# Kernel tuning notes

Hardware: AMD Instinct MI355X
Metric: run time of the kernel (lower is better)

The kernel has to match this reference:

```python
import jax, jax.numpy as jnp
import numpy as np

N = 50000      # nodes
E = 800000     # edges
F_IN = 256     # feat_dim
H = 256        # hidden dim (both layers)
L = 128        # latent dim
BN_EPS = 1e-5


def setup_inputs() -> dict:
    key = jax.random.key(0)
    ks = jax.random.split(key, 16)
    x = jax.random.normal(ks[0], (N, F_IN), dtype=jnp.float32)
    edge_index = jax.random.randint(ks[1], (2, E), 0, N, dtype=jnp.int32)
    s = 0.05
    return {
        "x": x,
        "edge_index": edge_index,
        "W0": s * jax.random.normal(ks[2], (F_IN, H), jnp.float32),
        "b0": jnp.zeros((H,), jnp.float32),
        "gamma0": jnp.ones((H,), jnp.float32),
        "beta0": jnp.zeros((H,), jnp.float32),
        "W1": s * jax.random.normal(ks[3], (H, H), jnp.float32),
        "b1": jnp.zeros((H,), jnp.float32),
        "gamma1": jnp.ones((H,), jnp.float32),
        "beta1": jnp.zeros((H,), jnp.float32),
        "W_mu": s * jax.random.normal(ks[4], (H, L), jnp.float32),
        "b_mu": jnp.zeros((L,), jnp.float32),
        "W_lv": s * jax.random.normal(ks[5], (H, L), jnp.float32),
        "b_lv": jnp.zeros((L,), jnp.float32),
    }


def _gcn_conv(h, src, dst, coef, W, b):
    # h' = W h, then symmetric-normalized scatter-add aggregation (PyG GCNConv)
    h = h @ W                                   # [N, H]
    msg = h[src] * coef                         # gather + scale, [E+N, H]
    out = jax.ops.segment_sum(msg, dst, num_segments=N)
    return out + b


def _bn(h, gamma, beta):
    # BatchNorm1d over node dimension (training-mode batch statistics)
    m = h.mean(axis=0)
    v = h.var(axis=0)
    return (h - m) * jax.lax.rsqrt(v + BN_EPS) * gamma + beta


def reference(x, edge_index, W0, b0, gamma0, beta0, W1, b1, gamma1, beta1,
              W_mu, b_mu, W_lv, b_lv):
    loops = jnp.arange(N, dtype=edge_index.dtype)
    src = jnp.concatenate([edge_index[0], loops])   # with self-loops
    dst = jnp.concatenate([edge_index[1], loops])
    deg = jax.ops.segment_sum(jnp.ones((E + N,), x.dtype), dst, num_segments=N)
    dinv = jnp.where(deg > 0, jax.lax.rsqrt(jnp.maximum(deg, 1.0)), 0.0)
    coef = (dinv[src] * dinv[dst])[:, None]          # [E+N, 1]

    h = jax.nn.relu(_bn(_gcn_conv(x, src, dst, coef, W0, b0), gamma0, beta0))
    h = jax.nn.relu(_bn(_gcn_conv(h, src, dst, coef, W1, b1), gamma1, beta1))
    # dropout is identity at inference
    mu = h @ W_mu + b_mu
    logvar = h @ W_lv + b_lv
    return mu, logvar
```

## Files before the change

kernel.cpp:

```cpp
#include <hip/hip_runtime.h>
#include <hip/hip_bf16.h>

#define NN 50000
#define NP 50001
#define NE 800000
#define FD 256
#define LD 128
#define BN_EPS 1e-5f
#define NEPAD (NE + 7 * NN + 16)

typedef __bf16 bf16_t;
typedef bf16_t bf16x8 __attribute__((ext_vector_type(8)));
typedef float f32x4 __attribute__((ext_vector_type(4)));
typedef float f32x2 __attribute__((ext_vector_type(2)));
typedef int i32x2 __attribute__((ext_vector_type(2)));
typedef int i32x4 __attribute__((ext_vector_type(4)));
typedef unsigned int u32x4 __attribute__((ext_vector_type(4)));
typedef unsigned short u16x8 __attribute__((ext_vector_type(8)));


__global__ __launch_bounds__(256) void k_count(const int* __restrict__ dst,
                                               int* __restrict__ cnt) {
  int i = blockIdx.x * blockDim.x + threadIdx.x;
  if (i < NE) atomicAdd(&cnt[dst[i]], 1);
}

__global__ __launch_bounds__(256) void k_scanA(const int* __restrict__ cnt,
                                               int* __restrict__ row_ptr,
                                               int* __restrict__ partials) {
  __shared__ int ws[4];
  int b = blockIdx.x, t = threadIdx.x;
  int base = b * 1024 + t * 4;
  int vals[4];
#pragma unroll
  for (int j = 0; j < 4; ++j)
    vals[j] = (base + j < NN) ? ((cnt[base + j] + 7) & ~7) : 0;
  int tsum = vals[0] + vals[1] + vals[2] + vals[3];
  int lane = t & 63, wid = t >> 6;
  int x = tsum;
#pragma unroll
  for (int off = 1; off < 64; off <<= 1) {
    int y = __shfl_up(x, off, 64);
    if (lane >= off) x += y;
  }
  if (lane == 63) ws[wid] = x;
  __syncthreads();
  int woff = 0;
  for (int w = 0; w < wid; ++w) woff += ws[w];
  int run = woff + x - tsum;
#pragma unroll
  for (int j = 0; j < 4; ++j) {
    if (base + j < NN) row_ptr[base + j] = run;
    run += vals[j];
  }
  if (t == 255) partials[b] = woff + x;
}

__global__ void k_scanB(int* __restrict__ partials, int* __restrict__ row_ptr,
                        int nblk) {
  int lane = threadIdx.x;
  int v = (lane < nblk) ? partials[lane] : 0;
  int x = v;
#pragma unroll
  for (int off = 1; off < 64; off <<= 1) {
    int y = __shfl_up(x, off, 64);
    if (lane >= off) x += y;
  }
  if (lane < nblk) partials[lane] = x - v;
  if (lane == nblk - 1) row_ptr[NN] = x;
}

__global__ __launch_bounds__(256) void k_scanC(int* __restrict__ row_ptr,
                                               const int* __restrict__ partials,
                                               const int* __restrict__ cnt,
                                               float* __restrict__ dinv,
                                               unsigned short* __restrict__ col,
                                               int* __restrict__ hist) {
  __shared__ int lh[64];
  int b = blockIdx.x, t = threadIdx.x;
  if (t < 64) lh[t] = 0;
  __syncthreads();
  int off = partials[b];
  int base = b * 1024 + t * 4;
#pragma unroll
  for (int j = 0; j < 4; ++j)
    if (base + j < NN) {
      int deg = cnt[base + j];
      int rp = row_ptr[base + j] + off;
      row_ptr[base + j] = rp;
      dinv[base + j] = rsqrtf(1.0f + (float)deg);
      int pd = (deg + 7) & ~7;
      for (int p = deg; p < pd; ++p) col[rp + p] = (unsigned short)NN;
      int it = pd >> 3;
      if (it > 63) it = 63;
      atomicAdd(&lh[it], 1);
    }
  __syncthreads();
  if (t < 64 && lh[t]) atomicAdd(&hist[t], lh[t]);
}

__global__ __launch_bounds__(256) void k_fill(const int* __restrict__ src,
                                              const int* __restrict__ dst,
                                              const int* __restrict__ row_ptr,
                                              int* __restrict__ cursor,
                                              unsigned short* __restrict__ col) {
  int i = blockIdx.x * blockDim.x + threadIdx.x;
  if (i < NE) {
    int d = dst[i];
    int p = atomicAdd(&cursor[d], 1);
    col[row_ptr[d] + p] = (unsigned short)src[i];
  }
}

__global__ void k_hscan(const int* __restrict__ hist, int* __restrict__ binoff) {
  int l = threadIdx.x;
  int v = hist[l];
  int x = v;
#pragma unroll
  for (int off = 1; off < 64; off <<= 1) {
    int y = __shfl_up(x, off, 64);
    if (l >= off) x += y;
  }
  binoff[l] = x - v;
}

__global__ __launch_bounds__(256) void k_order(
    const int* __restrict__ cnt, const int* __restrict__ row_ptr,
    const float* __restrict__ dinv, int* __restrict__ binoff,
    int* __restrict__ order, i32x2* __restrict__ desc,
    float* __restrict__ dinvp) {
  __shared__ int lcnt[64];
  __shared__ int gbase[64];
  int t = threadIdx.x;
  if (t < 64) lcnt[t] = 0;
  __syncthreads();
  int i = blockIdx.x * 256 + t;
  int it = 0, rloc = 0, pd = 0;
  bool valid = (i < NN);
  if (valid) {
    pd = (cnt[i] + 7) & ~7;
    it = pd >> 3;
    if (it > 63) it = 63;
    rloc = atomicAdd(&lcnt[it], 1);
  }
  __syncthreads();
  if (t < 64 && lcnt[t]) gbase[t] = atomicAdd(&binoff[t], lcnt[t]);
  __syncthreads();
  if (valid) {
    int p = gbase[it] + rloc;
    order[p] = i;
    int rp = row_ptr[i];
    desc[p] = (i32x2){rp, rp + pd};
    dinvp[p] = dinv[i];
  }
}

__global__ __launch_bounds__(256) void k_convw(
    const float* __restrict__ W0, const float* __restrict__ W1,
    const float* __restrict__ Wmu, const float* __restrict__ bmu,
    const float* __restrict__ Wlv, const float* __restrict__ blv,
    bf16_t* __restrict__ W0s, bf16_t* __restrict__ W1s,
    bf16_t* __restrict__ Whs, float* __restrict__ biash,
    bf16_t* __restrict__ g16, bf16_t* __restrict__ agg16) {
  int k = blockIdx.x, n = threadIdx.x;
  int chunk = (n >> 4) * 8 + (k >> 5);
  int slot = ((k >> 3) & 3) * 16 + (n & 15);
  int idx = chunk * 512 + slot * 8 + (k & 7);
  W0s[idx] = (bf16_t)W0[k * 256 + n];
  W1s[idx] = (bf16_t)W1[k * 256 + n];
  float wh = (n < 128) ? Wmu[k * 128 + n] : Wlv[k * 128 + (n - 128)];
  Whs[idx] = (bf16_t)wh;
  if (k == 0) biash[n] = (n < 128) ? bmu[n] : blv[n - 128];
  if (k == 1) {
    int ss = n >> 6, j = n & 63;
    g16[((size_t)ss * NP + NN) * 64 + j] = (bf16_t)0.f;
    agg16[((size_t)ss * NP + NN) * 64 + j] = (bf16_t)0.f;
  }
}

__global__ __launch_bounds__(256) void k_mgemm(
    const void* __restrict__ Ap, int a_f32, const bf16_t* __restrict__ Wswz,
    bf16_t* __restrict__ Cb, float* __restrict__ Cf, int M,
    const float* __restrict__ stats, const float* __restrict__ gamma,
    const float* __restrict__ beta, const float* __restrict__ row_scale,
    const float* __restrict__ col_bias, int split) {
  __shared__ bf16_t Ws[64 * 512];
  __shared__ float bnsc_l[256], bnsh_l[256];
  const int tid = threadIdx.x;
  const int half = blockIdx.y;
  {
    const bf16_t* srcW = Wswz + (size_t)half * 64 * 512;
    bf16x8 wraw[16];
#pragma unroll
    for (int i = 0; i < 16; ++i)
      wraw[i] = *(const bf16x8*)&srcW[(i * 256 + tid) * 8];
#pragma unroll
    for (int i = 0; i < 16; ++i) *(bf16x8*)&Ws[(i * 256 + tid) * 8] = wraw[i];
  }
  if (stats) {
    float mean = stats[tid] * (1.0f / NN);
    float var = stats[256 + tid] * (1.0f / NN) - mean * mean;
    float rs = rsqrtf(var + BN_EPS);
    float sc = gamma[tid] * rs;
    bnsc_l[tid] = sc;
    bnsh_l[tid] = beta[tid] - mean * sc;
  }
  __syncthreads();

  const int wave = tid >> 6, lane = tid & 63;
  const int m = lane & 15, q = lane >> 4;
  const int row0 = blockIdx.x * 128 + wave * 32;
  const int rg0 = row0 + m, rg1 = row0 + 16 + m;
  const int rc0 = rg0 < M ? rg0 : M - 1;
  const int rc1 = rg1 < M ? rg1 : M - 1;

  bf16x8 af[2][8];
  if (a_f32) {
    const float* p0 = (const float*)Ap + (size_t)rc0 * 256 + q * 8;
    const float* p1 = (const float*)Ap + (size_t)rc1 * 256 + q * 8;
#pragma unroll
    for (int g = 0; g < 2; ++g) {
      const float* p = g ? p1 : p0;
      float4 f0[8], f1[8];
#pragma unroll
      for (int kb = 0; kb < 8; ++kb) {
        f0[kb] = *(const float4*)(p + kb * 32);
        f1[kb] = *(const float4*)(p + kb * 32 + 4);
      }
#pragma unroll
      for (int kb = 0; kb < 8; ++kb) {
        bf16x8 fr;
        fr[0] = (bf16_t)f0[kb].x; fr[1] = (bf16_t)f0[kb].y;
        fr[2] = (bf16_t)f0[kb].z; fr[3] = (bf16_t)f0[kb].w;
        fr[4] = (bf16_t)f1[kb].x; fr[5] = (bf16_t)f1[kb].y;
        fr[6] = (bf16_t)f1[kb].z; fr[7] = (bf16_t)f1[kb].w;
        af[g][kb] = fr;
      }
    }
  } else {
    const bf16_t* pA = (const bf16_t*)Ap;
    bf16x8 raw[16];
#pragma unroll
    for (int kb = 0; kb < 8; ++kb) {
      raw[kb * 2 + 0] = *(const bf16x8*)&pA[((size_t)(kb >> 1) * NP + rc0) * 64 +
                                            (kb & 1) * 32 + q * 8];
      raw[kb * 2 + 1] = *(const bf16x8*)&pA[((size_t)(kb >> 1) * NP + rc1) * 64 +
                                            (kb & 1) * 32 + q * 8];
    }
#pragma unroll
    for (int kb = 0; kb < 8; ++kb) {
      float s[8], h[8];
      if (stats) {
        float4 s0 = *(const float4*)&bnsc_l[kb * 32 + q * 8];
        float4 s1 = *(const float4*)&bnsc_l[kb * 32 + q * 8 + 4];
        float4 h0 = *(const float4*)&bnsh_l[kb * 32 + q * 8];
        float4 h1 = *(const float4*)&bnsh_l[kb * 32 + q * 8 + 4];
        s[0] = s0.x; s[1] = s0.y; s[2] = s0.z; s[3] = s0.w;
        s[4] = s1.x; s[5] = s1.y; s[6] = s1.z; s[7] = s1.w;
        h[0] = h0.x; h[1] = h0.y; h[2] = h0.z; h[3] = h0.w;
        h[4] = h1.x; h[5] = h1.y; h[6] = h1.z; h[7] = h1.w;
      }
#pragma unroll
      for (int g = 0; g < 2; ++g) {
        bf16x8 r = raw[kb * 2 + g];
        bf16x8 fr;
#pragma unroll
        for (int j = 0; j < 8; ++j) {
          float v = (float)r[j];
          if (stats) v = fmaxf(fmaf(v, s[j], h[j]), 0.f);
          fr[j] = (bf16_t)v;
        }
        af[g][kb] = fr;
      }
    }
  }

  f32x4 acc[2][8] = {};
#pragma unroll
  for (int nt = 0; nt < 8; ++nt) {
#pragma unroll
    for (int kb = 0; kb < 8; ++kb) {
      bf16x8 b = *(const bf16x8*)&Ws[(nt * 8 + kb) * 512 + lane * 8];
      acc[0][nt] = __builtin_amdgcn_mfma_f32_16x16x32_bf16(af[0][kb], b,
                                                           acc[0][nt], 0, 0, 0);
      acc[1][nt] = __builtin_amdgcn_mfma_f32_16x16x32_bf16(af[1][kb], b,
                                                           acc[1][nt], 0, 0, 0);
    }
  }

#pragma unroll
  for (int g = 0; g < 2; ++g) {
#pragma unroll
    for (int r = 0; r < 4; ++r) {
      int row = row0 + g * 16 + q * 4 + r;
      if (row >= M) continue;
      float rs = row_scale ? row_scale[row] : 1.0f;
#pragma unroll
      for (int nt = 0; nt < 8; ++nt) {
        int col = half * 128 + nt * 16 + m;
        float v = acc[g][nt][r] * rs;
        if (col_bias) v += col_bias[col];
        if (Cb) {
          Cb[((size_t)(col >> 6) * NP + row) * 64 + (col & 63)] = (bf16_t)v;
        } else if (!split) {
          Cf[(size_t)row * 256 + col] = v;
        } else {
          if (col < 128)
            Cf[(size_t)row * 128 + col] = v;
          else
            Cf[(size_t)(M + row) * 128 + (col - 128)] = v;
        }
      }
    }
  }
}

#define ACCUM8(A, d)                                             \
  A[0] += (f32x2){__uint_as_float(d[0] << 16),                   \
                  __uint_as_float(d[0] & 0xffff0000u)};          \
  A[1] += (f32x2){__uint_as_float(d[1] << 16),                   \
                  __uint_as_float(d[1] & 0xffff0000u)};          \
  A[2] += (f32x2){__uint_as_float(d[2] << 16),                   \
                  __uint_as_float(d[2] & 0xffff0000u)};          \
  A[3] += (f32x2){__uint_as_float(d[3] << 16),                   \
                  __uint_as_float(d[3] & 0xffff0000u)};

__global__ __launch_bounds__(256) void k_spmm(
    const bf16_t* __restrict__ g, const int* __restrict__ order,
    const i32x2* __restrict__ desc, const unsigned short* __restrict__ col,
    const float* __restrict__ dinvp, bf16_t* __restrict__ out,
    float* __restrict__ stats) {
  __shared__ float sbuf[32][64];
  const int s = blockIdx.x & 3;
  const int grp = blockIdx.x >> 2;
  const int team = threadIdx.x >> 3, tl = threadIdx.x & 7;
  const int slotA = grp * 64 + team * 2;
  const u32x4* gu = (const u32x4*)(g + (size_t)s * NP * 64);
  float s1[8] = {}, s2[8] = {};
  if (slotA < NN) {
    f32x2 accA[4] = {}, accB[4] = {};
    i32x2 o2 = *(const i32x2*)&order[slotA];
    i32x4 d4 = *(const i32x4*)&desc[slotA];
    f32x2 dv2 = *(const f32x2*)&dinvp[slotA];
    int dstA = o2[0], dstB = o2[1];
    int bA = d4[0], eA = d4[1], bB = d4[2], eB = d4[3];
    {
      u32x4 dA = gu[(size_t)dstA * 8 + tl];
      u32x4 dB = gu[(size_t)dstB * 8 + tl];
      ACCUM8(accA, dA)
      ACCUM8(accB, dB)
    }
    u16x8 cA = {}, cB = {};
    if (bA < eA) cA = __builtin_nontemporal_load((const u16x8*)&col[bA]);
    if (bB < eB) cB = __builtin_nontemporal_load((const u16x8*)&col[bB]);
    while (bA < eA && bB < eB) {
      u32x4 wa0 = gu[(size_t)cA[0] * 8 + tl];
      u32x4 wa1 = gu[(size_t)cA[1] * 8 + tl];
      u32x4 wa2 = gu[(size_t)cA[2] * 8 + tl];
      u32x4 wa3 = gu[(size_t)cA[3] * 8 + tl];
      u32x4 wa4 = gu[(size_t)cA[4] * 8 + tl];
      u32x4 wa5 = gu[(size_t)cA[5] * 8 + tl];
      u32x4 wa6 = gu[(size_t)cA[6] * 8 + tl];
      u32x4 wa7 = gu[(size_t)cA[7] * 8 + tl];
      u32x4 wb0 = gu[(size_t)cB[0] * 8 + tl];
      u32x4 wb1 = gu[(size_t)cB[1] * 8 + tl];
      u32x4 wb2 = gu[(size_t)cB[2] * 8 + tl];
      u32x4 wb3 = gu[(size_t)cB[3] * 8 + tl];
      u32x4 wb4 = gu[(size_t)cB[4] * 8 + tl];
      u32x4 wb5 = gu[(size_t)cB[5] * 8 + tl];
      u32x4 wb6 = gu[(size_t)cB[6] * 8 + tl];
      u32x4 wb7 = gu[(size_t)cB[7] * 8 + tl];
      int bnA = bA + 8, bnB = bB + 8;
      u16x8 cnA = {}, cnB = {};
      if (bnA < eA) cnA = __builtin_nontemporal_load((const u16x8*)&col[bnA]);
      if (bnB < eB) cnB = __builtin_nontemporal_load((const u16x8*)&col[bnB]);
      ACCUM8(accA, wa0) ACCUM8(accA, wa1) ACCUM8(accA, wa2) ACCUM8(accA, wa3)
      ACCUM8(accA, wa4) ACCUM8(accA, wa5) ACCUM8(accA, wa6) ACCUM8(accA, wa7)
      ACCUM8(accB, wb0) ACCUM8(accB, wb1) ACCUM8(accB, wb2) ACCUM8(accB, wb3)
      ACCUM8(accB, wb4) ACCUM8(accB, wb5) ACCUM8(accB, wb6) ACCUM8(accB, wb7)
      cA = cnA;
      cB = cnB;
      bA = bnA;
      bB = bnB;
    }
    while (bA < eA) {
      u32x4 w0 = gu[(size_t)cA[0] * 8 + tl];
      u32x4 w1 = gu[(size_t)cA[1] * 8 + tl];
      u32x4 w2 = gu[(size_t)cA[2] * 8 + tl];
      u32x4 w3 = gu[(size_t)cA[3] * 8 + tl];
      u32x4 w4 = gu[(size_t)cA[4] * 8 + tl];
      u32x4 w5 = gu[(size_t)cA[5] * 8 + tl];
      u32x4 w6 = gu[(size_t)cA[6] * 8 + tl];
      u32x4 w7 = gu[(size_t)cA[7] * 8 + tl];
      int bn = bA + 8;
      u16x8 cn = {};
      if (bn < eA) cn = __builtin_nontemporal_load((const u16x8*)&col[bn]);
      ACCUM8(accA, w0) ACCUM8(accA, w1) ACCUM8(accA, w2) ACCUM8(accA, w3)
      ACCUM8(accA, w4) ACCUM8(accA, w5) ACCUM8(accA, w6) ACCUM8(accA, w7)
      cA = cn;
      bA = bn;
    }
    while (bB < eB) {
      u32x4 w0 = gu[(size_t)cB[0] * 8 + tl];
      u32x4 w1 = gu[(size_t)cB[1] * 8 + tl];
      u32x4 w2 = gu[(size_t)cB[2] * 8 + tl];
      u32x4 w3 = gu[(size_t)cB[3] * 8 + tl];
      u32x4 w4 = gu[(size_t)cB[4] * 8 + tl];
      u32x4 w5 = gu[(size_t)cB[5] * 8 + tl];
      u32x4 w6 = gu[(size_t)cB[6] * 8 + tl];
      u32x4 w7 = gu[(size_t)cB[7] * 8 + tl];
      int bn = bB + 8;
      u16x8 cn = {};
      if (bn < eB) cn = __builtin_nontemporal_load((const u16x8*)&col[bn]);
      ACCUM8(accB, w0) ACCUM8(accB, w1) ACCUM8(accB, w2) ACCUM8(accB, w3)
      ACCUM8(accB, w4) ACCUM8(accB, w5) ACCUM8(accB, w6) ACCUM8(accB, w7)
      cB = cn;
      bB = bn;
    }
    float dvA = dv2[0], dvB = dv2[1];
    bf16x8 ovA, ovB;
#pragma unroll
    for (int j = 0; j < 8; ++j) {
      ovA[j] = (bf16_t)(accA[j >> 1][j & 1] * dvA);
      ovB[j] = (bf16_t)(accB[j >> 1][j & 1] * dvB);
    }
    __builtin_nontemporal_store(
        ovA, (bf16x8*)&out[((size_t)s * NP + dstA) * 64 + (size_t)tl * 8]);
    __builtin_nontemporal_store(
        ovB, (bf16x8*)&out[((size_t)s * NP + dstB) * 64 + (size_t)tl * 8]);
#pragma unroll
    for (int j = 0; j < 8; ++j) {
      float va = (float)ovA[j], vb = (float)ovB[j];
      s1[j] += va + vb;
      s2[j] = fmaf(va, va, s2[j]);
      s2[j] = fmaf(vb, vb, s2[j]);
    }
  }
#pragma unroll
  for (int j = 0; j < 8; ++j) sbuf[team][tl * 8 + j] = s1[j];
  __syncthreads();
  if (threadIdx.x < 64) {
    float tot = 0.f;
#pragma unroll
    for (int w = 0; w < 32; ++w) tot += sbuf[w][threadIdx.x];
    atomicAdd(&stats[s * 64 + threadIdx.x], tot);
  }
  __syncthreads();
#pragma unroll
  for (int j = 0; j < 8; ++j) sbuf[team][tl * 8 + j] = s2[j];
  __syncthreads();
  if (threadIdx.x < 64) {
    float tot = 0.f;
#pragma unroll
    for (int w = 0; w < 32; ++w) tot += sbuf[w][threadIdx.x];
    atomicAdd(&stats[256 + s * 64 + threadIdx.x], tot);
  }
}

extern "C" void kernel_launch(void* const* d_in, const int* in_sizes, int n_in,
                              void* d_out, int out_size, void* d_ws, size_t ws_size,
                              hipStream_t stream) {
  const float* x = (const float*)d_in[0];
  const int* ei = (const int*)d_in[1];
  const int* esrc = ei;
  const int* edst = ei + NE;
  const float* W0 = (const float*)d_in[2];
  const float* gamma0 = (const float*)d_in[4];
  const float* beta0 = (const float*)d_in[5];
  const float* W1 = (const float*)d_in[6];
  const float* gamma1 = (const float*)d_in[8];
  const float* beta1 = (const float*)d_in[9];
  const float* W_mu = (const float*)d_in[10];
  const float* b_mu = (const float*)d_in[11];
  const float* W_lv = (const float*)d_in[12];
  const float* b_lv = (const float*)d_in[13];
  float* out = (float*)d_out;

  bf16_t* g16 = (bf16_t*)d_ws;
  bf16_t* agg16 = g16 + (size_t)4 * NP * 64;
  int* cnt = (int*)(agg16 + (size_t)4 * NP * 64);
  int* cursor = cnt + NN;
  float* statsAll = (float*)(cursor + NN);
  int* hist = (int*)(statsAll + 1024);
  int* binoff = hist + 64;
  float* dinv = (float*)(binoff + 64);
  float* biash = dinv + NN;
  bf16_t* W0s = (bf16_t*)(biash + 256);
  bf16_t* W1s = W0s + 256 * 256;
  bf16_t* Whs = W1s + 256 * 256;
  int* row_ptr = (int*)(Whs + 256 * 256);
  int* order = row_ptr + NN + 4;
  float* dinvp = (float*)(order + NN);
  i32x2* desc = (i32x2*)(dinvp + NN);
  unsigned short* col = (unsigned short*)(desc + NN);
  int* partials = (int*)(col + NEPAD);

  const int SCAN_BLKS = (NN + 1023) / 1024;

  hipMemsetAsync(cnt, 0, (2 * NN + 1024 + 128) * sizeof(int), stream);
  k_count<<<(NE + 255) / 256, 256, 0, stream>>>(edst, cnt);
  k_scanA<<<SCAN_BLKS, 256, 0, stream>>>(cnt, row_ptr, partials);
  k_scanB<<<1, 64, 0, stream>>>(partials, row_ptr, SCAN_BLKS);
  k_scanC<<<SCAN_BLKS, 256, 0, stream>>>(row_ptr, partials, cnt, dinv, col,
                                         hist);
  k_fill<<<(NE + 255) / 256, 256, 0, stream>>>(esrc, edst, row_ptr, cursor, col);
  k_hscan<<<1, 64, 0, stream>>>(hist, binoff);
  k_order<<<(NN + 255) / 256, 256, 0, stream>>>(cnt, row_ptr, dinv, binoff,
                                                order, desc, dinvp);
  k_convw<<<256, 256, 0, stream>>>(W0, W1, W_mu, b_mu, W_lv, b_lv, W0s, W1s,
                                   Whs, biash, g16, agg16);

  dim3 gg((NN + 127) / 128, 2);
  const int SPMM_BLKS = 4 * ((NN + 63) / 64);

  k_mgemm<<<gg, 256, 0, stream>>>(x, 1, W0s, g16, nullptr, NN, nullptr, nullptr,
                                  nullptr, dinv, nullptr, 0);
  k_spmm<<<SPMM_BLKS, 256, 0, stream>>>(g16, order, desc, col, dinvp, agg16,
                                        statsAll);

  k_mgemm<<<gg, 256, 0, stream>>>(agg16, 0, W1s, g16, nullptr, NN, statsAll,
                                  gamma0, beta0, dinv, nullptr, 0);
  k_spmm<<<SPMM_BLKS, 256, 0, stream>>>(g16, order, desc, col, dinvp, agg16,
                                        statsAll + 512);

  k_mgemm<<<gg, 256, 0, stream>>>(agg16, 0, Whs, nullptr, out, NN,
                                  statsAll + 512, gamma1, beta1, nullptr, biash,
                                  1);
}
```

Before: 410.8 us.

## Drop LDS weight staging in GEMM, halve row tile, fold hist scan into order

The GEMM kernel no longer stages its 64KB weight half in shared memory. Each lane now reads B fragments straight from global memory (L2-resident), and each wave handles 16 rows instead of 32, with twice as many blocks. This removes the large LDS footprint and the sync that limited occupancy, at the cost of repeated global/L2 weight reads and less reuse of each B fragment. Separately, the single-wave histogram scan kernel is folded into k_order, where every block recomputes the 64-bin prefix and uses a separate rank counter, which saves one launch.

```diff
diff --git a/kernel.cpp b/kernel.cpp
--- a/kernel.cpp
+++ b/kernel.cpp
@@ -112,27 +112,26 @@
   }
 }
 
-__global__ void k_hscan(const int* __restrict__ hist, int* __restrict__ binoff) {
-  int l = threadIdx.x;
-  int v = hist[l];
-  int x = v;
-#pragma unroll
-  for (int off = 1; off < 64; off <<= 1) {
-    int y = __shfl_up(x, off, 64);
-    if (l >= off) x += y;
-  }
-  binoff[l] = x - v;
-}
-
 __global__ __launch_bounds__(256) void k_order(
     const int* __restrict__ cnt, const int* __restrict__ row_ptr,
-    const float* __restrict__ dinv, int* __restrict__ binoff,
-    int* __restrict__ order, i32x2* __restrict__ desc,
+    const float* __restrict__ dinv, const int* __restrict__ hist,
+    int* __restrict__ rank, int* __restrict__ order, i32x2* __restrict__ desc,
     float* __restrict__ dinvp) {
   __shared__ int lcnt[64];
   __shared__ int gbase[64];
+  __shared__ int sc[64];
   int t = threadIdx.x;
-  if (t < 64) lcnt[t] = 0;
+  if (t < 64) {
+    lcnt[t] = 0;
+    int v = hist[t];
+    int x = v;
+#pragma unroll
+    for (int off = 1; off < 64; off <<= 1) {
+      int y = __shfl_up(x, off, 64);
+      if (t >= off) x += y;
+    }
+    sc[t] = x - v;
+  }
   __syncthreads();
   int i = blockIdx.x * 256 + t;
   int it = 0, rloc = 0, pd = 0;
@@ -144,7 +143,7 @@
     rloc = atomicAdd(&lcnt[it], 1);
   }
   __syncthreads();
-  if (t < 64 && lcnt[t]) gbase[t] = atomicAdd(&binoff[t], lcnt[t]);
+  if (t < 64 && lcnt[t]) gbase[t] = sc[t] + atomicAdd(&rank[t], lcnt[t]);
   __syncthreads();
   if (valid) {
     int p = gbase[it] + rloc;
@@ -184,19 +183,9 @@
     const float* __restrict__ stats, const float* __restrict__ gamma,
     const float* __restrict__ beta, const float* __restrict__ row_scale,
     const float* __restrict__ col_bias, int split) {
-  __shared__ bf16_t Ws[64 * 512];
   __shared__ float bnsc_l[256], bnsh_l[256];
   const int tid = threadIdx.x;
   const int half = blockIdx.y;
-  {
-    const bf16_t* srcW = Wswz + (size_t)half * 64 * 512;
-    bf16x8 wraw[16];
-#pragma unroll
-    for (int i = 0; i < 16; ++i)
-      wraw[i] = *(const bf16x8*)&srcW[(i * 256 + tid) * 8];
-#pragma unroll
-    for (int i = 0; i < 16; ++i) *(bf16x8*)&Ws[(i * 256 + tid) * 8] = wraw[i];
-  }
   if (stats) {
     float mean = stats[tid] * (1.0f / NN);
     float var = stats[256 + tid] * (1.0f / NN) - mean * mean;
@@ -204,49 +193,40 @@
     float sc = gamma[tid] * rs;
     bnsc_l[tid] = sc;
     bnsh_l[tid] = beta[tid] - mean * sc;
-  }
-  __syncthreads();
+    __syncthreads();
+  }
 
   const int wave = tid >> 6, lane = tid & 63;
   const int m = lane & 15, q = lane >> 4;
-  const int row0 = blockIdx.x * 128 + wave * 32;
-  const int rg0 = row0 + m, rg1 = row0 + 16 + m;
-  const int rc0 = rg0 < M ? rg0 : M - 1;
-  const int rc1 = rg1 < M ? rg1 : M - 1;
-
-  bf16x8 af[2][8];
+  const int row0 = blockIdx.x * 64 + wave * 16;
+  const int rg = row0 + m;
+  const int rc = rg < M ? rg : M - 1;
+
+  bf16x8 af[8];
   if (a_f32) {
-    const float* p0 = (const float*)Ap + (size_t)rc0 * 256 + q * 8;
-    const float* p1 = (const float*)Ap + (size_t)rc1 * 256 + q * 8;
-#pragma unroll
-    for (int g = 0; g < 2; ++g) {
-      const float* p = g ? p1 : p0;
-      float4 f0[8], f1[8];
-#pragma unroll
-      for (int kb = 0; kb < 8; ++kb) {
-        f0[kb] = *(const float4*)(p + kb * 32);
-        f1[kb] = *(const float4*)(p + kb * 32 + 4);
-      }
-#pragma unroll
-      for (int kb = 0; kb < 8; ++kb) {
-        bf16x8 fr;
-        fr[0] = (bf16_t)f0[kb].x; fr[1] = (bf16_t)f0[kb].y;
-        fr[2] = (bf16_t)f0[kb].z; fr[3] = (bf16_t)f0[kb].w;
-        fr[4] = (bf16_t)f1[kb].x; fr[5] = (bf16_t)f1[kb].y;
-        fr[6] = (bf16_t)f1[kb].z; fr[7] = (bf16_t)f1[kb].w;
-        af[g][kb] = fr;
-      }
+    const float* p = (const float*)Ap + (size_t)rc * 256 + q * 8;
+    float4 f0[8], f1[8];
+#pragma unroll
+    for (int kb = 0; kb < 8; ++kb) {
+      f0[kb] = *(const float4*)(p + kb * 32);
+      f1[kb] = *(const float4*)(p + kb * 32 + 4);
+    }
+#pragma unroll
+    for (int kb = 0; kb < 8; ++kb) {
+      bf16x8 fr;
+      fr[0] = (bf16_t)f0[kb].x; fr[1] = (bf16_t)f0[kb].y;
+      fr[2] = (bf16_t)f0[kb].z; fr[3] = (bf16_t)f0[kb].w;
+      fr[4] = (bf16_t)f1[kb].x; fr[5] = (bf16_t)f1[kb].y;
+      fr[6] = (bf16_t)f1[kb].z; fr[7] = (bf16_t)f1[kb].w;
+      af[kb] = fr;
     }
   } else {
     const bf16_t* pA = (const bf16_t*)Ap;
-    bf16x8 raw[16];
-#pragma unroll
-    for (int kb = 0; kb < 8; ++kb) {
-      raw[kb * 2 + 0] = *(const bf16x8*)&pA[((size_t)(kb >> 1) * NP + rc0) * 64 +
-                                            (kb & 1) * 32 + q * 8];
-      raw[kb * 2 + 1] = *(const bf16x8*)&pA[((size_t)(kb >> 1) * NP + rc1) * 64 +
-                                            (kb & 1) * 32 + q * 8];
-    }
+    bf16x8 raw[8];
+#pragma unroll
+    for (int kb = 0; kb < 8; ++kb)
+      raw[kb] = *(const bf16x8*)&pA[((size_t)(kb >> 1) * NP + rc) * 64 +
+                                    (kb & 1) * 32 + q * 8];
 #pragma unroll
     for (int kb = 0; kb < 8; ++kb) {
       float s[8], h[8];
@@ -260,56 +240,49 @@
         h[0] = h0.x; h[1] = h0.y; h[2] = h0.z; h[3] = h0.w;
         h[4] = h1.x; h[5] = h1.y; h[6] = h1.z; h[7] = h1.w;
       }
-#pragma unroll
-      for (int g = 0; g < 2; ++g) {
-        bf16x8 r = raw[kb * 2 + g];
-        bf16x8 fr;
-#pragma unroll
-        for (int j = 0; j < 8; ++j) {
-          float v = (float)r[j];
-          if (stats) v = fmaxf(fmaf(v, s[j], h[j]), 0.f);
-          fr[j] = (bf16_t)v;
-        }
-        af[g][kb] = fr;
+      bf16x8 r = raw[kb];
+      bf16x8 fr;
+#pragma unroll
+      for (int j = 0; j < 8; ++j) {
+        float v = (float)r[j];
+        if (stats) v = fmaxf(fmaf(v, s[j], h[j]), 0.f);
+        fr[j] = (bf16_t)v;
       }
-    }
-  }
-
-  f32x4 acc[2][8] = {};
+      af[kb] = fr;
+    }
+  }
+
+  const bf16_t* Wb = Wswz + (size_t)half * 64 * 512 + lane * 8;
+  f32x4 acc[8] = {};
 #pragma unroll
   for (int nt = 0; nt < 8; ++nt) {
 #pragma unroll
     for (int kb = 0; kb < 8; ++kb) {
-      bf16x8 b = *(const bf16x8*)&Ws[(nt * 8 + kb) * 512 + lane * 8];
-      acc[0][nt] = __builtin_amdgcn_mfma_f32_16x16x32_bf16(af[0][kb], b,
-                                                           acc[0][nt], 0, 0, 0);
-      acc[1][nt] = __builtin_amdgcn_mfma_f32_16x16x32_bf16(af[1][kb], b,
-                                                           acc[1][nt], 0, 0, 0);
-    }
-  }
-
-#pragma unroll
-  for (int g = 0; g < 2; ++g) {
-#pragma unroll
-    for (int r = 0; r < 4; ++r) {
-      int row = row0 + g * 16 + q * 4 + r;
-      if (row >= M) continue;
-      float rs = row_scale ? row_scale[row] : 1.0f;
-#pragma unroll
-      for (int nt = 0; nt < 8; ++nt) {
-        int col = half * 128 + nt * 16 + m;
-        float v = acc[g][nt][r] * rs;
-        if (col_bias) v += col_bias[col];
-        if (Cb) {
-          Cb[((size_t)(col >> 6) * NP + row) * 64 + (col & 63)] = (bf16_t)v;
-        } else if (!split) {
-          Cf[(size_t)row * 256 + col] = v;
-        } else {
-          if (col < 128)
-            Cf[(size_t)row * 128 + col] = v;
-          else
-            Cf[(size_t)(M + row) * 128 + (col - 128)] = v;
-        }
+      bf16x8 b = *(const bf16x8*)&Wb[(nt * 8 + kb) * 512];
+      acc[nt] =
+          __builtin_amdgcn_mfma_f32_16x16x32_bf16(af[kb], b, acc[nt], 0, 0, 0);
+    }
+  }
+
+#pragma unroll
+  for (int r = 0; r < 4; ++r) {
+    int row = row0 + q * 4 + r;
+    if (row >= M) continue;
+    float rs = row_scale ? row_scale[row] : 1.0f;
+#pragma unroll
+    for (int nt = 0; nt < 8; ++nt) {
+      int col = half * 128 + nt * 16 + m;
+      float v = acc[nt][r] * rs;
+      if (col_bias) v += col_bias[col];
+      if (Cb) {
+        Cb[((size_t)(col >> 6) * NP + row) * 64 + (col & 63)] = (bf16_t)v;
+      } else if (!split) {
+        Cf[(size_t)row * 256 + col] = v;
+      } else {
+        if (col < 128)
+          Cf[(size_t)row * 128 + col] = v;
+        else
+          Cf[(size_t)(M + row) * 128 + (col - 128)] = v;
       }
     }
   }
@@ -482,8 +455,8 @@
   int* cursor = cnt + NN;
   float* statsAll = (float*)(cursor + NN);
   int* hist = (int*)(statsAll + 1024);
-  int* binoff = hist + 64;
-  float* dinv = (float*)(binoff + 64);
+  int* rank = hist + 64;
+  float* dinv = (float*)(rank + 64);
   float* biash = dinv + NN;
   bf16_t* W0s = (bf16_t*)(biash + 256);
   bf16_t* W1s = W0s + 256 * 256;
@@ -504,13 +477,12 @@
   k_scanC<<<SCAN_BLKS, 256, 0, stream>>>(row_ptr, partials, cnt, dinv, col,
                                          hist);
   k_fill<<<(NE + 255) / 256, 256, 0, stream>>>(esrc, edst, row_ptr, cursor, col);
-  k_hscan<<<1, 64, 0, stream>>>(hist, binoff);
-  k_order<<<(NN + 255) / 256, 256, 0, stream>>>(cnt, row_ptr, dinv, binoff,
+  k_order<<<(NN + 255) / 256, 256, 0, stream>>>(cnt, row_ptr, dinv, hist, rank,
                                                 order, desc, dinvp);
   k_convw<<<256, 256, 0, stream>>>(W0, W1, W_mu, b_mu, W_lv, b_lv, W0s, W1s,
                                    Whs, biash, g16, agg16);
 
-  dim3 gg((NN + 127) / 128, 2);
+  dim3 gg((NN + 63) / 64, 2);
   const int SPMM_BLKS = 4 * ((NN + 63) / 64);
 
   k_mgemm<<<gg, 256, 0, stream>>>(x, 1, W0s, g16, nullptr, NN, nullptr, nullptr,
```

After: 402.3 us. -2.1%, faster.
